# Kernel optimization log

Hardware: AMD Instinct MI355X
Metric: run time of the kernel (lower is better)

## Reference

```python
import jax, jax.numpy as jnp
import numpy as np

WINDOW_SIZE = 512
CAUSAL = True

def _sliding_window_mask(seq_len, window_size, causal):
    i = jnp.arange(seq_len)[:, None]
    j = jnp.arange(seq_len)[None, :]
    mask = (j >= i - window_size + 1) & (j <= i)
    if causal:
        mask = mask & (j <= i)
    return mask  # [S, S] bool, True = attend


def setup_inputs() -> dict:
    key = jax.random.key(0)
    k1, k2, k3 = jax.random.split(key, 3)
    B, S, D = 16, 4096, 64
    q = jax.random.normal(k1, (B, S, D), dtype=jnp.float32)
    k = jax.random.normal(k2, (B, S, D), dtype=jnp.float32)
    v = jax.random.normal(k3, (B, S, D), dtype=jnp.float32)
    return {"q": q, "k": k, "v": v}


def reference(q, k, v):
    B, S, D = q.shape
    scale = D ** -0.5
    mask = _sliding_window_mask(S, WINDOW_SIZE, CAUSAL)  # [S, S]
    scores = jnp.einsum("bqd,bkd->bqk", q, k) * scale    # [B, S, S]
    mask_value = -jnp.finfo(scores.dtype).max
    scores = jnp.where(mask[None, :, :], scores, mask_value)
    attn = jax.nn.softmax(scores, axis=-1)
    out = jnp.einsum("bqk,bkd->bqd", attn, v)            # [B, S, D]
    return out
```

## Files before the change

### kernel.cpp

```cpp
#include <hip/hip_runtime.h>

#define BATCH 16
#define SEQ   4096
#define DIM   64
#define WIN   512

constexpr int BM = 256;
constexpr int BN = 64;
constexpr int NTHREADS = 1024;
constexpr int KS = DIM + 8;
constexpr int VS = BN + 4;
constexpr float QSCALE  = 0.125f * 1.44269504088896340736f;
constexpr float MASKVAL = -3.0e38f;

typedef _Float16 f16x2 __attribute__((ext_vector_type(2)));
typedef _Float16 f16x4 __attribute__((ext_vector_type(4)));
typedef _Float16 f16x8 __attribute__((ext_vector_type(8)));
typedef float    f32x4 __attribute__((ext_vector_type(4)));

__device__ __forceinline__ f16x2 pk2(float a, float b) {
    return __builtin_bit_cast(f16x2, __builtin_amdgcn_cvt_pkrtz(a, b));
}

__device__ __forceinline__ void stage_kv(_Float16* __restrict__ Ksh, _Float16* __restrict__ Vsh,
                                         const float4& kv, const float4& vv,
                                         int row, int c4) {
    union { f16x4 v; f16x2 h[2]; } uk;
    uk.h[0] = pk2(kv.x, kv.y);
    uk.h[1] = pk2(kv.z, kv.w);
    *(f16x4*)&Ksh[row * KS + c4] = uk.v;
    Vsh[(c4 + 0) * VS + row] = (_Float16)vv.x;
    Vsh[(c4 + 1) * VS + row] = (_Float16)vv.y;
    Vsh[(c4 + 2) * VS + row] = (_Float16)vv.z;
    Vsh[(c4 + 3) * VS + row] = (_Float16)vv.w;
}

__global__ __launch_bounds__(NTHREADS)
void swa_kernel(const float* __restrict__ qg, const float* __restrict__ kg,
                const float* __restrict__ vg, float* __restrict__ outg) {
    __shared__ __align__(16) char smem[(BN * KS + DIM * VS) * 2];
    _Float16* Ksh = (_Float16*)smem;
    _Float16* Vsh = (_Float16*)(smem + BN * KS * 2);

    const int tid  = threadIdx.x;
    const int lane = tid & 63;
    const int wave = tid >> 6;
    const int lr   = lane & 15;
    const int quad = lane >> 4;

    const int b     = blockIdx.y;
    const int qblk  = blockIdx.x;
    const int qrow0 = qblk * BM;
    const int wr0   = qrow0 + wave * 16;
    const int q     = wr0 + lr;

    const float* qb = qg + (size_t)b * SEQ * DIM;
    const float* kb = kg + (size_t)b * SEQ * DIM;
    const float* vb = vg + (size_t)b * SEQ * DIM;
    float*       ob = outg + (size_t)b * SEQ * DIM;

    const int row0 = tid >> 4;
    const int c4   = (tid & 15) * 4;

    const float* qp = qb + (size_t)q * DIM + quad * 8;
    const float4 a0 = *(const float4*)(qp + 0);
    const float4 a1 = *(const float4*)(qp + 4);
    const float4 a2 = *(const float4*)(qp + 32);
    const float4 a3 = *(const float4*)(qp + 36);
    union { f16x8 v; f16x2 h[4]; } uq0, uq1;
    uq0.h[0] = pk2(a0.x * QSCALE, a0.y * QSCALE);
    uq0.h[1] = pk2(a0.z * QSCALE, a0.w * QSCALE);
    uq0.h[2] = pk2(a1.x * QSCALE, a1.y * QSCALE);
    uq0.h[3] = pk2(a1.z * QSCALE, a1.w * QSCALE);
    uq1.h[0] = pk2(a2.x * QSCALE, a2.y * QSCALE);
    uq1.h[1] = pk2(a2.z * QSCALE, a2.w * QSCALE);
    uq1.h[2] = pk2(a3.x * QSCALE, a3.y * QSCALE);
    uq1.h[3] = pk2(a3.z * QSCALE, a3.w * QSCALE);
    const f16x8 qf0 = uq0.v, qf1 = uq1.v;

    f32x4 o[4];
    #pragma unroll
    for (int mi = 0; mi < 4; ++mi) o[mi] = (f32x4){0.f, 0.f, 0.f, 0.f};
    float m_run = -1e30f, l_run = 0.f;

    const int t0 = (qrow0 > (WIN - 1)) ? (qrow0 - (WIN - 1)) >> 6 : 0;
    const int t1 = (qrow0 + BM - 1) >> 6;

    {
        const size_t g0 = (size_t)(t0 * BN + row0) * DIM + c4;
        stage_kv(Ksh, Vsh, *(const float4*)&kb[g0], *(const float4*)&vb[g0], row0, c4);
    }
    __syncthreads();

    for (int t = t0; t <= t1; ++t) {
        const bool have_next = (t < t1);
        float4 kpre, vpre;
        if (have_next) {
            const size_t g = (size_t)((t + 1) * BN + row0) * DIM + c4;
            kpre = *(const float4*)&kb[g];
            vpre = *(const float4*)&vb[g];
        }

        const int kbase = t * BN;
        const bool active = (kbase + BN - 1 >= wr0 - (WIN - 1)) && (kbase <= wr0 + 15);
        if (active) {
            f32x4 sc[4];
            #pragma unroll
            for (int mt = 0; mt < 4; ++mt) {
                const f16x8 kf0 = *(const f16x8*)&Ksh[(mt * 16 + lr) * KS + quad * 8];
                const f16x8 kf1 = *(const f16x8*)&Ksh[(mt * 16 + lr) * KS + 32 + quad * 8];
                f32x4 s = (f32x4){0.f, 0.f, 0.f, 0.f};
                s = __builtin_amdgcn_mfma_f32_16x16x32_f16(kf0, qf0, s, 0, 0, 0);
                s = __builtin_amdgcn_mfma_f32_16x16x32_f16(kf1, qf1, s, 0, 0, 0);
                sc[mt] = s;
            }

            const bool edge = (kbase < wr0 + 15 - (WIN - 1)) || (kbase + BN - 1 > wr0);
            if (edge) {
                #pragma unroll
                for (int mt = 0; mt < 4; ++mt) {
                    #pragma unroll
                    for (int r = 0; r < 4; ++r) {
                        const int key = kbase + mt * 16 + quad * 4 + r;
                        sc[mt][r] = ((unsigned)(q - key) < (unsigned)WIN) ? sc[mt][r] : MASKVAL;
                    }
                }
            }

            float mt_ = MASKVAL;
            #pragma unroll
            for (int mtile = 0; mtile < 4; ++mtile)
                #pragma unroll
                for (int r = 0; r < 4; ++r) mt_ = fmaxf(mt_, sc[mtile][r]);
            mt_ = fmaxf(mt_, __shfl_xor(mt_, 16));
            mt_ = fmaxf(mt_, __shfl_xor(mt_, 32));
            const float mn    = fmaxf(m_run, mt_);
            const float alpha = exp2f(m_run - mn);
            m_run = mn;

            f16x4 pb[4];
            float ls = 0.f;
            #pragma unroll
            for (int nt = 0; nt < 4; ++nt) {
                const float p0 = exp2f(sc[nt][0] - mn);
                const float p1 = exp2f(sc[nt][1] - mn);
                const float p2 = exp2f(sc[nt][2] - mn);
                const float p3 = exp2f(sc[nt][3] - mn);
                ls += (p0 + p1) + (p2 + p3);
                union { f16x4 v; f16x2 h[2]; } up;
                up.h[0] = pk2(p0, p1);
                up.h[1] = pk2(p2, p3);
                pb[nt] = up.v;
            }
            l_run = l_run * alpha + ls;
            #pragma unroll
            for (int mi = 0; mi < 4; ++mi) o[mi] = o[mi] * alpha;

            #pragma unroll
            for (int nt = 0; nt < 4; ++nt) {
                #pragma unroll
                for (int mi = 0; mi < 4; ++mi) {
                    const f16x4 vf = *(const f16x4*)&Vsh[(mi * 16 + lr) * VS + nt * 16 + quad * 4];
                    o[mi] = __builtin_amdgcn_mfma_f32_16x16x16f16(vf, pb[nt], o[mi], 0, 0, 0);
                }
            }
        }

        __builtin_amdgcn_s_barrier();
        if (have_next) {
            stage_kv(Ksh, Vsh, kpre, vpre, row0, c4);
        }
        __syncthreads();
    }

    l_run += __shfl_xor(l_run, 16);
    l_run += __shfl_xor(l_run, 32);
    const float inv = 1.0f / l_run;
    #pragma unroll
    for (int mi = 0; mi < 4; ++mi) {
        float4 st;
        st.x = o[mi][0] * inv; st.y = o[mi][1] * inv;
        st.z = o[mi][2] * inv; st.w = o[mi][3] * inv;
        *(float4*)&ob[(size_t)q * DIM + mi * 16 + quad * 4] = st;
    }
}

extern "C" void kernel_launch(void* const* d_in, const int* in_sizes, int n_in,
                              void* d_out, int out_size, void* d_ws, size_t ws_size,
                              hipStream_t stream) {
    (void)in_sizes; (void)n_in; (void)out_size; (void)d_ws; (void)ws_size;
    const float* q = (const float*)d_in[0];
    const float* k = (const float*)d_in[1];
    const float* v = (const float*)d_in[2];
    float* out = (float*)d_out;
    dim3 grid(SEQ / BM, BATCH);
    swa_kernel<<<grid, dim3(NTHREADS), 0, stream>>>(q, k, v, out);
}
```

Measured before the change: 110.7 us.

## Switch to 32x32x16 MFMA tiles with smaller 256-thread blocks

Replaces the 16x16 MFMA formulation with 32x32x16 f16 MFMAs, so each wave handles 32 query rows and accumulates into 16-wide fp32 vectors. Block size drops from 1024 to 256 threads with 128 query rows per block. Each thread now stages a 16-column strip of one key row, and the K smem padding changes. P fragments are rearranged between lane halves with cross-lane shuffles to match the B operand layout. This aims at higher MFMA throughput and better occupancy, at the cost of shuffle overhead and more redundant K/V window loads per query because the blocks are smaller.

Result: slower. 118.9 us (+7.4%).

```diff
diff --git a/kernel.cpp b/kernel.cpp
--- a/kernel.cpp
+++ b/kernel.cpp
@@ -5,34 +5,46 @@
 #define DIM   64
 #define WIN   512
 
-constexpr int BM = 256;
+constexpr int BM = 128;
 constexpr int BN = 64;
-constexpr int NTHREADS = 1024;
-constexpr int KS = DIM + 8;
+constexpr int NTHREADS = 256;
+constexpr int KS = DIM + 4;
 constexpr int VS = BN + 4;
 constexpr float QSCALE  = 0.125f * 1.44269504088896340736f;
 constexpr float MASKVAL = -3.0e38f;
 
-typedef _Float16 f16x2 __attribute__((ext_vector_type(2)));
-typedef _Float16 f16x4 __attribute__((ext_vector_type(4)));
-typedef _Float16 f16x8 __attribute__((ext_vector_type(8)));
-typedef float    f32x4 __attribute__((ext_vector_type(4)));
+typedef _Float16 f16x2  __attribute__((ext_vector_type(2)));
+typedef _Float16 f16x4  __attribute__((ext_vector_type(4)));
+typedef _Float16 f16x8  __attribute__((ext_vector_type(8)));
+typedef float    f32x16 __attribute__((ext_vector_type(16)));
 
 __device__ __forceinline__ f16x2 pk2(float a, float b) {
     return __builtin_bit_cast(f16x2, __builtin_amdgcn_cvt_pkrtz(a, b));
 }
+__device__ __forceinline__ int pk2i(float a, float b) {
+    return __builtin_bit_cast(int, __builtin_amdgcn_cvt_pkrtz(a, b));
+}
+__device__ __forceinline__ f16x8 ld8(const _Float16* p) {
+    union { f16x8 v; f16x4 h[2]; } u;
+    u.h[0] = *(const f16x4*)p;
+    u.h[1] = *(const f16x4*)(p + 4);
+    return u.v;
+}
 
 __device__ __forceinline__ void stage_kv(_Float16* __restrict__ Ksh, _Float16* __restrict__ Vsh,
-                                         const float4& kv, const float4& vv,
-                                         int row, int c4) {
-    union { f16x4 v; f16x2 h[2]; } uk;
-    uk.h[0] = pk2(kv.x, kv.y);
-    uk.h[1] = pk2(kv.z, kv.w);
-    *(f16x4*)&Ksh[row * KS + c4] = uk.v;
-    Vsh[(c4 + 0) * VS + row] = (_Float16)vv.x;
-    Vsh[(c4 + 1) * VS + row] = (_Float16)vv.y;
-    Vsh[(c4 + 2) * VS + row] = (_Float16)vv.z;
-    Vsh[(c4 + 3) * VS + row] = (_Float16)vv.w;
+                                         const float4* kvv, const float4* vvv,
+                                         int krow, int dbase) {
+    #pragma unroll
+    for (int s = 0; s < 4; ++s) {
+        union { f16x4 v; f16x2 h[2]; } uk;
+        uk.h[0] = pk2(kvv[s].x, kvv[s].y);
+        uk.h[1] = pk2(kvv[s].z, kvv[s].w);
+        *(f16x4*)&Ksh[krow * KS + dbase + 4 * s] = uk.v;
+        Vsh[(dbase + 4 * s + 0) * VS + krow] = (_Float16)vvv[s].x;
+        Vsh[(dbase + 4 * s + 1) * VS + krow] = (_Float16)vvv[s].y;
+        Vsh[(dbase + 4 * s + 2) * VS + krow] = (_Float16)vvv[s].z;
+        Vsh[(dbase + 4 * s + 3) * VS + krow] = (_Float16)vvv[s].w;
+    }
 }
 
 __global__ __launch_bounds__(NTHREADS)
@@ -45,143 +57,160 @@
     const int tid  = threadIdx.x;
     const int lane = tid & 63;
     const int wave = tid >> 6;
-    const int lr   = lane & 15;
-    const int quad = lane >> 4;
+    const int ql   = lane & 31;
+    const int h    = lane >> 5;
 
     const int b     = blockIdx.y;
     const int qblk  = blockIdx.x;
     const int qrow0 = qblk * BM;
-    const int wr0   = qrow0 + wave * 16;
-    const int q     = wr0 + lr;
+    const int wq0   = qrow0 + wave * 32;
+    const int q     = wq0 + ql;
 
     const float* qb = qg + (size_t)b * SEQ * DIM;
     const float* kb = kg + (size_t)b * SEQ * DIM;
     const float* vb = vg + (size_t)b * SEQ * DIM;
     float*       ob = outg + (size_t)b * SEQ * DIM;
 
-    const int row0 = tid >> 4;
-    const int c4   = (tid & 15) * 4;
-
-    const float* qp = qb + (size_t)q * DIM + quad * 8;
-    const float4 a0 = *(const float4*)(qp + 0);
-    const float4 a1 = *(const float4*)(qp + 4);
-    const float4 a2 = *(const float4*)(qp + 32);
-    const float4 a3 = *(const float4*)(qp + 36);
-    union { f16x8 v; f16x2 h[4]; } uq0, uq1;
-    uq0.h[0] = pk2(a0.x * QSCALE, a0.y * QSCALE);
-    uq0.h[1] = pk2(a0.z * QSCALE, a0.w * QSCALE);
-    uq0.h[2] = pk2(a1.x * QSCALE, a1.y * QSCALE);
-    uq0.h[3] = pk2(a1.z * QSCALE, a1.w * QSCALE);
-    uq1.h[0] = pk2(a2.x * QSCALE, a2.y * QSCALE);
-    uq1.h[1] = pk2(a2.z * QSCALE, a2.w * QSCALE);
-    uq1.h[2] = pk2(a3.x * QSCALE, a3.y * QSCALE);
-    uq1.h[3] = pk2(a3.z * QSCALE, a3.w * QSCALE);
-    const f16x8 qf0 = uq0.v, qf1 = uq1.v;
-
-    f32x4 o[4];
+    const int krow  = lane;
+    const int dbase = wave * 16;
+
+    f16x8 qf[4];
     #pragma unroll
-    for (int mi = 0; mi < 4; ++mi) o[mi] = (f32x4){0.f, 0.f, 0.f, 0.f};
+    for (int kc = 0; kc < 4; ++kc) {
+        const float* qp = qb + (size_t)q * DIM + kc * 16 + h * 8;
+        const float4 x = *(const float4*)(qp + 0);
+        const float4 y = *(const float4*)(qp + 4);
+        union { f16x8 v; f16x2 p[4]; } u;
+        u.p[0] = pk2(x.x * QSCALE, x.y * QSCALE);
+        u.p[1] = pk2(x.z * QSCALE, x.w * QSCALE);
+        u.p[2] = pk2(y.x * QSCALE, y.y * QSCALE);
+        u.p[3] = pk2(y.z * QSCALE, y.w * QSCALE);
+        qf[kc] = u.v;
+    }
+
+    f32x16 o0 = (f32x16)(0.f), o1 = (f32x16)(0.f);
     float m_run = -1e30f, l_run = 0.f;
 
     const int t0 = (qrow0 > (WIN - 1)) ? (qrow0 - (WIN - 1)) >> 6 : 0;
     const int t1 = (qrow0 + BM - 1) >> 6;
 
     {
-        const size_t g0 = (size_t)(t0 * BN + row0) * DIM + c4;
-        stage_kv(Ksh, Vsh, *(const float4*)&kb[g0], *(const float4*)&vb[g0], row0, c4);
+        float4 kv[4], vv[4];
+        const float* kp = kb + (size_t)(t0 * BN + krow) * DIM + dbase;
+        const float* vp = vb + (size_t)(t0 * BN + krow) * DIM + dbase;
+        #pragma unroll
+        for (int s = 0; s < 4; ++s) {
+            kv[s] = *(const float4*)(kp + 4 * s);
+            vv[s] = *(const float4*)(vp + 4 * s);
+        }
+        stage_kv(Ksh, Vsh, kv, vv, krow, dbase);
     }
     __syncthreads();
 
     for (int t = t0; t <= t1; ++t) {
         const bool have_next = (t < t1);
-        float4 kpre, vpre;
+        float4 kpre[4], vpre[4];
         if (have_next) {
-            const size_t g = (size_t)((t + 1) * BN + row0) * DIM + c4;
-            kpre = *(const float4*)&kb[g];
-            vpre = *(const float4*)&vb[g];
+            const float* kp = kb + (size_t)((t + 1) * BN + krow) * DIM + dbase;
+            const float* vp = vb + (size_t)((t + 1) * BN + krow) * DIM + dbase;
+            #pragma unroll
+            for (int s = 0; s < 4; ++s) {
+                kpre[s] = *(const float4*)(kp + 4 * s);
+                vpre[s] = *(const float4*)(vp + 4 * s);
+            }
         }
 
         const int kbase = t * BN;
-        const bool active = (kbase + BN - 1 >= wr0 - (WIN - 1)) && (kbase <= wr0 + 15);
+        const bool active = (kbase <= wq0 + 31) && (kbase + BN - 1 >= wq0 - (WIN - 1));
         if (active) {
-            f32x4 sc[4];
-            #pragma unroll
-            for (int mt = 0; mt < 4; ++mt) {
-                const f16x8 kf0 = *(const f16x8*)&Ksh[(mt * 16 + lr) * KS + quad * 8];
-                const f16x8 kf1 = *(const f16x8*)&Ksh[(mt * 16 + lr) * KS + 32 + quad * 8];
-                f32x4 s = (f32x4){0.f, 0.f, 0.f, 0.f};
-                s = __builtin_amdgcn_mfma_f32_16x16x32_f16(kf0, qf0, s, 0, 0, 0);
-                s = __builtin_amdgcn_mfma_f32_16x16x32_f16(kf1, qf1, s, 0, 0, 0);
-                sc[mt] = s;
-            }
-
-            const bool edge = (kbase < wr0 + 15 - (WIN - 1)) || (kbase + BN - 1 > wr0);
+            f32x16 s0 = (f32x16)(0.f), s1 = (f32x16)(0.f);
+            #pragma unroll
+            for (int kc = 0; kc < 4; ++kc) {
+                const int off = kc * 16 + h * 8;
+                const f16x8 a0 = ld8(&Ksh[(ql) * KS + off]);
+                const f16x8 a1 = ld8(&Ksh[(32 + ql) * KS + off]);
+                s0 = __builtin_amdgcn_mfma_f32_32x32x16_f16(a0, qf[kc], s0, 0, 0, 0);
+                s1 = __builtin_amdgcn_mfma_f32_32x32x16_f16(a1, qf[kc], s1, 0, 0, 0);
+            }
+
+            const bool edge = (kbase < wq0 + 31 - (WIN - 1)) || (kbase + BN - 1 > wq0);
             if (edge) {
                 #pragma unroll
-                for (int mt = 0; mt < 4; ++mt) {
-                    #pragma unroll
-                    for (int r = 0; r < 4; ++r) {
-                        const int key = kbase + mt * 16 + quad * 4 + r;
-                        sc[mt][r] = ((unsigned)(q - key) < (unsigned)WIN) ? sc[mt][r] : MASKVAL;
-                    }
+                for (int r = 0; r < 16; ++r) {
+                    const int k0 = kbase + (r & 3) + 8 * (r >> 2) + 4 * h;
+                    s0[r] = ((unsigned)(q - k0) < (unsigned)WIN) ? s0[r] : MASKVAL;
+                    const int k1 = k0 + 32;
+                    s1[r] = ((unsigned)(q - k1) < (unsigned)WIN) ? s1[r] : MASKVAL;
                 }
             }
 
             float mt_ = MASKVAL;
             #pragma unroll
-            for (int mtile = 0; mtile < 4; ++mtile)
-                #pragma unroll
-                for (int r = 0; r < 4; ++r) mt_ = fmaxf(mt_, sc[mtile][r]);
-            mt_ = fmaxf(mt_, __shfl_xor(mt_, 16));
+            for (int r = 0; r < 16; ++r) mt_ = fmaxf(mt_, fmaxf(s0[r], s1[r]));
             mt_ = fmaxf(mt_, __shfl_xor(mt_, 32));
             const float mn    = fmaxf(m_run, mt_);
             const float alpha = exp2f(m_run - mn);
             m_run = mn;
 
-            f16x4 pb[4];
+            f32x16 p0, p1;
             float ls = 0.f;
             #pragma unroll
-            for (int nt = 0; nt < 4; ++nt) {
-                const float p0 = exp2f(sc[nt][0] - mn);
-                const float p1 = exp2f(sc[nt][1] - mn);
-                const float p2 = exp2f(sc[nt][2] - mn);
-                const float p3 = exp2f(sc[nt][3] - mn);
-                ls += (p0 + p1) + (p2 + p3);
-                union { f16x4 v; f16x2 h[2]; } up;
-                up.h[0] = pk2(p0, p1);
-                up.h[1] = pk2(p2, p3);
-                pb[nt] = up.v;
+            for (int r = 0; r < 16; ++r) {
+                p0[r] = exp2f(s0[r] - mn);
+                p1[r] = exp2f(s1[r] - mn);
+                ls += p0[r] + p1[r];
             }
             l_run = l_run * alpha + ls;
             #pragma unroll
-            for (int mi = 0; mi < 4; ++mi) o[mi] = o[mi] * alpha;
-
-            #pragma unroll
-            for (int nt = 0; nt < 4; ++nt) {
-                #pragma unroll
-                for (int mi = 0; mi < 4; ++mi) {
-                    const f16x4 vf = *(const f16x4*)&Vsh[(mi * 16 + lr) * VS + nt * 16 + quad * 4];
-                    o[mi] = __builtin_amdgcn_mfma_f32_16x16x16f16(vf, pb[nt], o[mi], 0, 0, 0);
-                }
+            for (int r = 0; r < 16; ++r) { o0[r] *= alpha; o1[r] *= alpha; }
+
+            #pragma unroll
+            for (int kc = 0; kc < 4; ++kc) {
+                const f32x16 pm = (kc < 2) ? p0 : p1;
+                const int base = 8 * (kc & 1);
+                const int A0 = pk2i(pm[base + 0], pm[base + 1]);
+                const int A1 = pk2i(pm[base + 2], pm[base + 3]);
+                const int B0 = pk2i(pm[base + 4], pm[base + 5]);
+                const int B1 = pk2i(pm[base + 6], pm[base + 7]);
+                const int s0_ = h ? A0 : B0;
+                const int s1_ = h ? A1 : B1;
+                const int r0 = __shfl_xor(s0_, 32);
+                const int r1 = __shfl_xor(s1_, 32);
+                union { f16x8 v; int i[4]; } pb;
+                pb.i[0] = h ? r0 : A0;
+                pb.i[1] = h ? r1 : A1;
+                pb.i[2] = h ? B0 : r0;
+                pb.i[3] = h ? B1 : r1;
+                const int off = kc * 16 + h * 8;
+                const f16x8 vf0 = ld8(&Vsh[(ql) * VS + off]);
+                const f16x8 vf1 = ld8(&Vsh[(32 + ql) * VS + off]);
+                o0 = __builtin_amdgcn_mfma_f32_32x32x16_f16(vf0, pb.v, o0, 0, 0, 0);
+                o1 = __builtin_amdgcn_mfma_f32_32x32x16_f16(vf1, pb.v, o1, 0, 0, 0);
             }
         }
 
         __builtin_amdgcn_s_barrier();
         if (have_next) {
-            stage_kv(Ksh, Vsh, kpre, vpre, row0, c4);
+            stage_kv(Ksh, Vsh, kpre, vpre, krow, dbase);
         }
         __syncthreads();
     }
 
-    l_run += __shfl_xor(l_run, 16);
     l_run += __shfl_xor(l_run, 32);
     const float inv = 1.0f / l_run;
     #pragma unroll
-    for (int mi = 0; mi < 4; ++mi) {
-        float4 st;
-        st.x = o[mi][0] * inv; st.y = o[mi][1] * inv;
-        st.z = o[mi][2] * inv; st.w = o[mi][3] * inv;
-        *(float4*)&ob[(size_t)q * DIM + mi * 16 + quad * 4] = st;
+    for (int mt = 0; mt < 2; ++mt) {
+        const f32x16 ov = mt ? o1 : o0;
+        #pragma unroll
+        for (int g = 0; g < 4; ++g) {
+            const int d = mt * 32 + 8 * g + 4 * h;
+            float4 st;
+            st.x = ov[4 * g + 0] * inv;
+            st.y = ov[4 * g + 1] * inv;
+            st.z = ov[4 * g + 2] * inv;
+            st.w = ov[4 * g + 3] * inv;
+            *(float4*)&ob[(size_t)q * DIM + d] = st;
+        }
     }
 }
 
```

## Halve query block to 128 rows and XOR-swizzle K/V shared memory

Applied to the files above, without the earlier changes.

Query tile shrinks from 256 to 128 rows with 512 threads, so twice as many blocks run per batch and each block iterates over fewer extra key tiles. Padded shared-memory layouts are replaced with XOR-swizzled unpadded layouts for K and transposed V, and each thread now stages 8 contiguous elements of one key row per tile. The goal is fewer LDS bank conflicts and better occupancy or load balance. The cost is more redundant K/V loads across the overlapping windows of smaller query blocks.

After: 110.5 us. Within noise of the previous version (-0.1%).

```diff
diff --git a/kernel.cpp b/kernel.cpp
--- a/kernel.cpp
+++ b/kernel.cpp
@@ -5,11 +5,9 @@
 #define DIM   64
 #define WIN   512
 
-constexpr int BM = 256;
+constexpr int BM = 128;
 constexpr int BN = 64;
-constexpr int NTHREADS = 1024;
-constexpr int KS = DIM + 8;
-constexpr int VS = BN + 4;
+constexpr int NTHREADS = 512;
 constexpr float QSCALE  = 0.125f * 1.44269504088896340736f;
 constexpr float MASKVAL = -3.0e38f;
 
@@ -23,24 +21,31 @@
 }
 
 __device__ __forceinline__ void stage_kv(_Float16* __restrict__ Ksh, _Float16* __restrict__ Vsh,
-                                         const float4& kv, const float4& vv,
-                                         int row, int c4) {
-    union { f16x4 v; f16x2 h[2]; } uk;
-    uk.h[0] = pk2(kv.x, kv.y);
-    uk.h[1] = pk2(kv.z, kv.w);
-    *(f16x4*)&Ksh[row * KS + c4] = uk.v;
-    Vsh[(c4 + 0) * VS + row] = (_Float16)vv.x;
-    Vsh[(c4 + 1) * VS + row] = (_Float16)vv.y;
-    Vsh[(c4 + 2) * VS + row] = (_Float16)vv.z;
-    Vsh[(c4 + 3) * VS + row] = (_Float16)vv.w;
+                                         const float4* kv, const float4* vv,
+                                         int krow, int w) {
+    union { f16x8 v; f16x2 h[4]; } uk;
+    uk.h[0] = pk2(kv[0].x, kv[0].y);
+    uk.h[1] = pk2(kv[0].z, kv[0].w);
+    uk.h[2] = pk2(kv[1].x, kv[1].y);
+    uk.h[3] = pk2(kv[1].z, kv[1].w);
+    *(f16x8*)&Ksh[krow * 64 + ((w ^ (krow & 7)) * 8)] = uk.v;
+    const int jb = krow >> 2, e = krow & 3;
+    #pragma unroll
+    for (int s = 0; s < 2; ++s) {
+        const float* vf = (const float*)&vv[s];
+        #pragma unroll
+        for (int j = 0; j < 4; ++j) {
+            const int d = 8 * w + 4 * s + j;
+            Vsh[d * 64 + ((jb ^ (d & 15)) * 4) + e] = (_Float16)vf[j];
+        }
+    }
 }
 
 __global__ __launch_bounds__(NTHREADS)
 void swa_kernel(const float* __restrict__ qg, const float* __restrict__ kg,
                 const float* __restrict__ vg, float* __restrict__ outg) {
-    __shared__ __align__(16) char smem[(BN * KS + DIM * VS) * 2];
-    _Float16* Ksh = (_Float16*)smem;
-    _Float16* Vsh = (_Float16*)(smem + BN * KS * 2);
+    __shared__ __align__(16) _Float16 Ksh[BN * 64];
+    __shared__ __align__(16) _Float16 Vsh[DIM * 64];
 
     const int tid  = threadIdx.x;
     const int lane = tid & 63;
@@ -59,8 +64,7 @@
     const float* vb = vg + (size_t)b * SEQ * DIM;
     float*       ob = outg + (size_t)b * SEQ * DIM;
 
-    const int row0 = tid >> 4;
-    const int c4   = (tid & 15) * 4;
+    const int krow = lane;
 
     const float* qp = qb + (size_t)q * DIM + quad * 8;
     const float4 a0 = *(const float4*)(qp + 0);
@@ -87,18 +91,27 @@
     const int t1 = (qrow0 + BM - 1) >> 6;
 
     {
-        const size_t g0 = (size_t)(t0 * BN + row0) * DIM + c4;
-        stage_kv(Ksh, Vsh, *(const float4*)&kb[g0], *(const float4*)&vb[g0], row0, c4);
+        float4 kv[2], vv[2];
+        const float* kp = kb + (size_t)(t0 * BN + krow) * DIM + 8 * wave;
+        const float* vp = vb + (size_t)(t0 * BN + krow) * DIM + 8 * wave;
+        kv[0] = *(const float4*)(kp + 0);
+        kv[1] = *(const float4*)(kp + 4);
+        vv[0] = *(const float4*)(vp + 0);
+        vv[1] = *(const float4*)(vp + 4);
+        stage_kv(Ksh, Vsh, kv, vv, krow, wave);
     }
     __syncthreads();
 
     for (int t = t0; t <= t1; ++t) {
         const bool have_next = (t < t1);
-        float4 kpre, vpre;
+        float4 kpre[2], vpre[2];
         if (have_next) {
-            const size_t g = (size_t)((t + 1) * BN + row0) * DIM + c4;
-            kpre = *(const float4*)&kb[g];
-            vpre = *(const float4*)&vb[g];
+            const float* kp = kb + (size_t)((t + 1) * BN + krow) * DIM + 8 * wave;
+            const float* vp = vb + (size_t)((t + 1) * BN + krow) * DIM + 8 * wave;
+            kpre[0] = *(const float4*)(kp + 0);
+            kpre[1] = *(const float4*)(kp + 4);
+            vpre[0] = *(const float4*)(vp + 0);
+            vpre[1] = *(const float4*)(vp + 4);
         }
 
         const int kbase = t * BN;
@@ -107,8 +120,9 @@
             f32x4 sc[4];
             #pragma unroll
             for (int mt = 0; mt < 4; ++mt) {
-                const f16x8 kf0 = *(const f16x8*)&Ksh[(mt * 16 + lr) * KS + quad * 8];
-                const f16x8 kf1 = *(const f16x8*)&Ksh[(mt * 16 + lr) * KS + 32 + quad * 8];
+                const int row = mt * 16 + lr;
+                const f16x8 kf0 = *(const f16x8*)&Ksh[row * 64 + ((quad       ^ (lr & 7)) * 8)];
+                const f16x8 kf1 = *(const f16x8*)&Ksh[row * 64 + (((4 | quad) ^ (lr & 7)) * 8)];
                 f32x4 s = (f32x4){0.f, 0.f, 0.f, 0.f};
                 s = __builtin_amdgcn_mfma_f32_16x16x32_f16(kf0, qf0, s, 0, 0, 0);
                 s = __builtin_amdgcn_mfma_f32_16x16x32_f16(kf1, qf1, s, 0, 0, 0);
@@ -160,7 +174,8 @@
             for (int nt = 0; nt < 4; ++nt) {
                 #pragma unroll
                 for (int mi = 0; mi < 4; ++mi) {
-                    const f16x4 vf = *(const f16x4*)&Vsh[(mi * 16 + lr) * VS + nt * 16 + quad * 4];
+                    const int d = mi * 16 + lr;
+                    const f16x4 vf = *(const f16x4*)&Vsh[d * 64 + (((4 * nt + quad) ^ lr) * 4)];
                     o[mi] = __builtin_amdgcn_mfma_f32_16x16x16f16(vf, pb[nt], o[mi], 0, 0, 0);
                 }
             }
@@ -168,7 +183,7 @@
 
         __builtin_amdgcn_s_barrier();
         if (have_next) {
-            stage_kv(Ksh, Vsh, kpre, vpre, row0, c4);
+            stage_kv(Ksh, Vsh, kpre, vpre, krow, wave);
         }
         __syncthreads();
     }
```
